# Kernel optimization log

Hardware: AMD Instinct MI355X
Metric: run time of the kernel (lower is better)

## Reference

```python
import jax, jax.numpy as jnp
import numpy as np

D_MODEL = 1024
NUM_HEADS = 16
DEPTH = D_MODEL // NUM_HEADS


def setup_inputs() -> dict:
    key = jax.random.key(0)
    ks = jax.random.split(key, 9)
    s = 1.0 / np.sqrt(D_MODEL)
    x = jax.random.normal(ks[0], (2, 2048, D_MODEL), dtype=jnp.float32)
    def lin(kw, kb):
        W = jax.random.uniform(kw, (D_MODEL, D_MODEL), jnp.float32, -s, s)
        b = jax.random.uniform(kb, (D_MODEL,), jnp.float32, -s, s)
        return W, b
    Wq, bq = lin(ks[1], ks[2])
    Wk, bk = lin(ks[3], ks[4])
    Wv, bv = lin(ks[5], ks[6])
    Wo, bo = lin(ks[7], ks[8])
    return {"x": x, "Wq": Wq, "bq": bq, "Wk": Wk, "bk": bk,
            "Wv": Wv, "bv": bv, "Wo": Wo, "bo": bo}


def reference(x, Wq, bq, Wk, bk, Wv, bv, Wo, bo):
    B, T, _ = x.shape
    # projections; weights stored as [in, out] (torch Linear applies x @ W.T; here W is already [in,out])
    def split_heads(y):
        return y.reshape(B, T, NUM_HEADS, DEPTH).transpose(0, 2, 1, 3)  # [B,H,T,D]
    Q = split_heads(x @ Wq + bq)
    K = split_heads(x @ Wk + bk)
    V = split_heads(x @ Wv + bv)
    scale = 1.0 / jnp.sqrt(jnp.asarray(DEPTH, dtype=x.dtype))
    scores = jnp.einsum('bhqd,bhkd->bhqk', Q, K) * scale  # [B,H,T,T]
    attn = jax.nn.softmax(scores, axis=-1)
    out = jnp.einsum('bhqk,bhkd->bhqd', attn, V)  # [B,H,T,D]
    out = out.transpose(0, 2, 1, 3).reshape(B, T, D_MODEL)
    return out @ Wo + bo
```

## Files before the change

kernel.cpp:

```cpp
#include <hip/hip_runtime.h>
#include <hip/hip_bf16.h>

typedef unsigned short ushort_t;
typedef short s8v __attribute__((ext_vector_type(8)));
typedef float f4v __attribute__((ext_vector_type(4)));
typedef float f16v __attribute__((ext_vector_type(16)));

#define DM 1024
#define TT 2048
#define NH 16
#define DH 64
#define QSCALE 0.18033688011112042f

__device__ __forceinline__ ushort_t f2bf(float f) {
  union { float f; unsigned u; } v; v.f = f;
  unsigned u = v.u;
  return (ushort_t)((u + 0x7fffu + ((u >> 16) & 1u)) >> 16);
}

__device__ __forceinline__ unsigned pk2bf(float a, float b) {
  union { __hip_bfloat162 h; unsigned u; } v;
  v.h = __float22bfloat162_rn(float2{a, b});
  return v.u;
}

__device__ __forceinline__ f16v splat16(float x) {
  f16v v;
#pragma unroll
  for (int i = 0; i < 16; i++) v[i] = x;
  return v;
}

__device__ __forceinline__ void gll16(const void* g, const void* l) {
  __builtin_amdgcn_global_load_lds(
      (const __attribute__((address_space(1))) unsigned int*)g,
      (__attribute__((address_space(3))) unsigned int*)l, 16, 0, 0);
}

__global__ __launch_bounds__(256) void wtrans4_kernel(const float* __restrict__ W0,
                                                      const float* __restrict__ W1,
                                                      const float* __restrict__ W2,
                                                      const float* __restrict__ W3,
                                                      ushort_t* __restrict__ dst) {
  __shared__ float tile[32][33];
  const int z = blockIdx.z;
  const float* W = z == 0 ? W0 : (z == 1 ? W1 : (z == 2 ? W2 : W3));
  ushort_t* Wt = dst + (size_t)z * DM * DM;
  int tx = threadIdx.x & 31, ty = threadIdx.x >> 5;
  int n0 = blockIdx.x * 32, k0 = blockIdx.y * 32;
#pragma unroll
  for (int i = 0; i < 4; i++)
    tile[ty + i * 8][tx] = W[(size_t)(k0 + ty + i * 8) * DM + n0 + tx];
  __syncthreads();
#pragma unroll
  for (int i = 0; i < 4; i++)
    Wt[(size_t)(n0 + ty + i * 8) * DM + k0 + tx] = f2bf(tile[tx][ty + i * 8]);
}

__global__ __launch_bounds__(256) void xconv_kernel(const float* __restrict__ x,
                                                    ushort_t* __restrict__ xb) {
  int i = blockIdx.x * 256 + threadIdx.x;
  const float4* p = (const float4*)x + (size_t)i * 2;
  float4 a = p[0], b = p[1];
  union { ushort_t s[8]; uint4 u; } r;
  r.s[0] = f2bf(a.x); r.s[1] = f2bf(a.y); r.s[2] = f2bf(a.z); r.s[3] = f2bf(a.w);
  r.s[4] = f2bf(b.x); r.s[5] = f2bf(b.y); r.s[6] = f2bf(b.z); r.s[7] = f2bf(b.w);
  *((uint4*)xb + i) = r.u;
}

__global__ __launch_bounds__(256) void vtrans_kernel(const ushort_t* __restrict__ V,
                                                     ushort_t* __restrict__ Vt) {
  __shared__ ushort_t Ls[64][72];
  const int t = threadIdx.x;
  const int t0 = blockIdx.x * 64, bh = blockIdx.y;
  const ushort_t* Vb = V + (size_t)bh * TT * DH;
  ushort_t* Vtb = Vt + (size_t)bh * DH * TT;
#pragma unroll
  for (int c = t; c < 512; c += 256) {
    int tt = c & 63, dch = c >> 6;
    union { uint4 u; ushort_t s[8]; } uu;
    uu.u = *(const uint4*)&Vb[(size_t)(t0 + tt) * DH + dch * 8];
#pragma unroll
    for (int i = 0; i < 8; i++) Ls[dch * 8 + i][tt] = uu.s[i];
  }
  __syncthreads();
#pragma unroll
  for (int c = t; c < 512; c += 256) {
    int d = c >> 3, tch = c & 7;
    uint4 u = *(const uint4*)&Ls[d][tch * 8];
    *(uint4*)&Vtb[(size_t)d * TT + t0 + tch * 8] = u;
  }
}

template <int MT, int MODE>
__global__ __launch_bounds__(256) void gemm_bt(
    const ushort_t* __restrict__ A, const ushort_t* __restrict__ Bt,
    const float* __restrict__ bias0, const float* __restrict__ bias1,
    const float* __restrict__ bias2,
    ushort_t* __restrict__ qo, ushort_t* __restrict__ ko, ushort_t* __restrict__ vo,
    float* __restrict__ co) {
  constexpr int TM = MT * 32;
  __shared__ __align__(16) ushort_t Asm[2][TM * 32];
  __shared__ __align__(16) ushort_t Bsm[2][128 * 32];
  const int m0 = blockIdx.x * TM, n0 = blockIdx.y * 128;
  const int t = threadIdx.x, lane = t & 63;
  const int wid = t >> 6, wr = wid >> 1, wc = wid & 1;
  const ushort_t* Ab = A + (size_t)m0 * DM;
  const ushort_t* Bb = Bt + (size_t)n0 * DM;

  f4v zero = {0.f, 0.f, 0.f, 0.f};
  f4v acc[MT][4];
#pragma unroll
  for (int i = 0; i < MT; i++)
#pragma unroll
    for (int j = 0; j < 4; j++) acc[i][j] = zero;

  const int r0 = t >> 2;
  const int csw = ((t & 3) ^ ((r0 >> 1) & 3)) * 8;
  const int rr = lane & 15, q8 = lane >> 4;

#define GSTAGE(kb, bb)                                                      \
  do {                                                                      \
    int k0_ = (kb) * 32 + csw;                                              \
    gll16(Ab + (size_t)r0 * DM + k0_, &Asm[bb][t * 8]);                     \
    if constexpr (MT == 4)                                                  \
      gll16(Ab + (size_t)(r0 + 64) * DM + k0_, &Asm[bb][(t + 256) * 8]);    \
    gll16(Bb + (size_t)r0 * DM + k0_, &Bsm[bb][t * 8]);                     \
    gll16(Bb + (size_t)(r0 + 64) * DM + k0_, &Bsm[bb][(t + 256) * 8]);      \
  } while (0)

  GSTAGE(0, 0);
  for (int kb = 0; kb < 32; ++kb) {
    const int cur = kb & 1;
    if (kb < 31) {
      GSTAGE(kb + 1, cur ^ 1);
      if constexpr (MT == 4)
        asm volatile("s_waitcnt vmcnt(4)" ::: "memory");
      else
        asm volatile("s_waitcnt vmcnt(3)" ::: "memory");
    } else {
      asm volatile("s_waitcnt vmcnt(0)" ::: "memory");
    }
    __builtin_amdgcn_s_barrier();
    __builtin_amdgcn_sched_barrier(0);

    s8v af[MT], bf_[4];
#pragma unroll
    for (int mt = 0; mt < MT; mt++) {
      int row = wr * (MT * 16) + mt * 16 + rr;
      af[mt] = *(const s8v*)&Asm[cur][row * 32 + ((q8 ^ ((row >> 1) & 3)) << 3)];
    }
#pragma unroll
    for (int nt = 0; nt < 4; nt++) {
      int row = wc * 64 + nt * 16 + rr;
      bf_[nt] = *(const s8v*)&Bsm[cur][row * 32 + ((q8 ^ ((row >> 1) & 3)) << 3)];
    }
    __builtin_amdgcn_s_setprio(1);
#pragma unroll
    for (int mt = 0; mt < MT; mt++)
#pragma unroll
      for (int nt = 0; nt < 4; nt++)
        acc[mt][nt] =
            __builtin_amdgcn_mfma_f32_16x16x32_bf16(af[mt], bf_[nt], acc[mt][nt], 0, 0, 0);
    __builtin_amdgcn_s_setprio(0);
    __builtin_amdgcn_sched_barrier(0);
    __builtin_amdgcn_s_barrier();
  }
#undef GSTAGE

  const int col_l = lane & 15, row_q = (lane >> 4) * 4;
  if (MODE == 0) {
    const int qkv = n0 >> 10;
    const float* bias = qkv == 0 ? bias0 : (qkv == 1 ? bias1 : bias2);
    ushort_t* dst = qkv == 0 ? qo : (qkv == 1 ? ko : vo);
    const float sc = qkv == 0 ? QSCALE : 1.0f;
    const int nb = n0 & 1023;
#pragma unroll
    for (int nt = 0; nt < 4; nt++) {
      int gc = nb + wc * 64 + nt * 16 + col_l;
      float bv_ = bias[gc];
      int hh = gc >> 6, d = gc & 63;
#pragma unroll
      for (int mt = 0; mt < MT; mt++) {
#pragma unroll
        for (int j = 0; j < 4; j++) {
          int r = m0 + wr * (MT * 16) + mt * 16 + row_q + j;
          int bb = r >> 11, tt_ = r & 2047;
          dst[(((size_t)(bb * NH + hh)) * TT + tt_) * DH + d] = f2bf((acc[mt][nt][j] + bv_) * sc);
        }
      }
    }
  } else {
#pragma unroll
    for (int nt = 0; nt < 4; nt++) {
      int gc = n0 + wc * 64 + nt * 16 + col_l;
      float bv_ = bias0[gc];
#pragma unroll
      for (int mt = 0; mt < MT; mt++) {
#pragma unroll
        for (int j = 0; j < 4; j++) {
          int r = m0 + wr * (MT * 16) + mt * 16 + row_q + j;
          co[(size_t)r * DM + gc] = acc[mt][nt][j] + bv_;
        }
      }
    }
  }
}

__global__ __launch_bounds__(256, 2) void attn_kernel(const ushort_t* __restrict__ Q,
                                                      const ushort_t* __restrict__ K,
                                                      const ushort_t* __restrict__ Vt,
                                                      ushort_t* __restrict__ O) {
  __shared__ __align__(16) ushort_t Ksm[2][64 * 64];
  __shared__ __align__(16) ushort_t Vsm[2][64 * 64];

  const int b_lin = blockIdx.x + (blockIdx.y << 4);
  const int xcd = b_lin & 7, n = b_lin >> 3;
  const int bh = (xcd << 2) | (n >> 4);
  const int qt = n & 15;
  const int b = bh >> 4, h = bh & 15;
  const int t = threadIdx.x, lane = t & 63, wid = t >> 6;
  const int lo = lane & 31, hi = lane >> 5;
  const ushort_t* Qb = Q + ((size_t)bh * TT + qt * 128 + wid * 32) * DH;
  const ushort_t* Kb = K + (size_t)bh * TT * DH;
  const ushort_t* Vb = Vt + (size_t)bh * DH * TT;

  s8v qf[4];
#pragma unroll
  for (int ks = 0; ks < 4; ks++)
    qf[ks] = *(const s8v*)&Qb[lo * 64 + ks * 16 + hi * 8];

  f16v oacc[2];
  oacc[0] = splat16(0.f);
  oacc[1] = splat16(0.f);
  float mreg = 0.f, lreg = 0.f;

  const int c0r = t >> 3, c0s = ((t & 7) ^ (c0r & 7)) * 8;
  const int c1 = t + 256;
  const int c1r = c1 >> 3, c1s = ((t & 7) ^ (c1r & 7)) * 8;

#define STAGE(tv, bb)                                              \
  do {                                                             \
    int kv0_ = (tv) * 64;                                          \
    gll16(&Kb[(size_t)(kv0_ + c0r) * DH + c0s], &Ksm[bb][t * 8]);  \
    gll16(&Vb[(size_t)c0r * TT + kv0_ + c0s], &Vsm[bb][t * 8]);    \
    gll16(&Kb[(size_t)(kv0_ + c1r) * DH + c1s], &Ksm[bb][c1 * 8]); \
    gll16(&Vb[(size_t)c1r * TT + kv0_ + c1s], &Vsm[bb][c1 * 8]);   \
  } while (0)

  STAGE(0, 0);
  for (int tv = 0; tv < 32; ++tv) {
    const int cur = tv & 1;
    if (tv < 31) {
      STAGE(tv + 1, cur ^ 1);
      asm volatile("s_waitcnt vmcnt(4)" ::: "memory");
    } else {
      asm volatile("s_waitcnt vmcnt(0)" ::: "memory");
    }
    __builtin_amdgcn_s_barrier();
    __builtin_amdgcn_sched_barrier(0);

    f16v st0 = splat16(-mreg), st1 = splat16(-mreg);
    __builtin_amdgcn_s_setprio(1);
#pragma unroll
    for (int ks = 0; ks < 4; ks++) {
      int ch = ((ks * 2 + hi) ^ (lo & 7)) << 3;
      s8v kf0 = *(const s8v*)&Ksm[cur][lo * 64 + ch];
      s8v kf1 = *(const s8v*)&Ksm[cur][(32 + lo) * 64 + ch];
      st0 = __builtin_amdgcn_mfma_f32_32x32x16_bf16(kf0, qf[ks], st0, 0, 0, 0);
      st1 = __builtin_amdgcn_mfma_f32_32x32x16_bf16(kf1, qf[ks], st1, 0, 0, 0);
    }
    __builtin_amdgcn_s_setprio(0);

    float pmax = -1e30f;
#pragma unroll
    for (int i = 0; i < 16; i++) pmax = fmaxf(pmax, fmaxf(st0[i], st1[i]));
    pmax = fmaxf(pmax, __shfl_xor(pmax, 32, 64));
    if (!__all(pmax <= 8.0f)) {
      float delta = fmaxf(pmax, 0.f);
      float corr = __builtin_amdgcn_exp2f(-delta);
      mreg += delta;
      st0 -= delta;
      st1 -= delta;
      lreg *= corr;
      oacc[0] *= corr;
      oacc[1] *= corr;
    }
#pragma unroll
    for (int i = 0; i < 16; i++) {
      st0[i] = __builtin_amdgcn_exp2f(st0[i]);
      st1[i] = __builtin_amdgcn_exp2f(st1[i]);
    }
    float ps = 0.f;
#pragma unroll
    for (int i = 0; i < 16; i++) ps += st0[i] + st1[i];
    ps += __shfl_xor(ps, 32, 64);
    lreg += ps;

    s8v pb[4];
#pragma unroll
    for (int kt = 0; kt < 2; kt++) {
#pragma unroll
      for (int s = 0; s < 2; s++) {
        unsigned w0, w1, w2, w3;
        if (kt == 0) {
          w0 = pk2bf(st0[8 * s + 0], st0[8 * s + 1]);
          w1 = pk2bf(st0[8 * s + 2], st0[8 * s + 3]);
          w2 = pk2bf(st0[8 * s + 4], st0[8 * s + 5]);
          w3 = pk2bf(st0[8 * s + 6], st0[8 * s + 7]);
        } else {
          w0 = pk2bf(st1[8 * s + 0], st1[8 * s + 1]);
          w1 = pk2bf(st1[8 * s + 2], st1[8 * s + 3]);
          w2 = pk2bf(st1[8 * s + 4], st1[8 * s + 5]);
          w3 = pk2bf(st1[8 * s + 6], st1[8 * s + 7]);
        }
        asm volatile("v_permlane32_swap_b32 %0, %1" : "+v"(w0), "+v"(w2));
        asm volatile("v_permlane32_swap_b32 %0, %1" : "+v"(w1), "+v"(w3));
        union { unsigned u[4]; s8v v; } pw;
        pw.u[0] = w0; pw.u[1] = w1; pw.u[2] = w2; pw.u[3] = w3;
        pb[kt * 2 + s] = pw.v;
      }
    }

    __builtin_amdgcn_s_setprio(1);
#pragma unroll
    for (int ks = 0; ks < 4; ks++) {
      int ch = ((ks * 2 + hi) ^ (lo & 7)) << 3;
      s8v vf0 = *(const s8v*)&Vsm[cur][lo * 64 + ch];
      s8v vf1 = *(const s8v*)&Vsm[cur][(32 + lo) * 64 + ch];
      oacc[0] = __builtin_amdgcn_mfma_f32_32x32x16_bf16(vf0, pb[ks], oacc[0], 0, 0, 0);
      oacc[1] = __builtin_amdgcn_mfma_f32_32x32x16_bf16(vf1, pb[ks], oacc[1], 0, 0, 0);
    }
    __builtin_amdgcn_s_setprio(0);

    __builtin_amdgcn_sched_barrier(0);
    __builtin_amdgcn_s_barrier();
  }
#undef STAGE

  float linv = 1.0f / lreg;
  ushort_t* Osm = &Ksm[0][0] + wid * 2048;
#pragma unroll
  for (int dt = 0; dt < 2; dt++) {
#pragma unroll
    for (int r = 0; r < 8; r++) {
      int dbase = ((2 * r) & 3) + 8 * ((2 * r) >> 2);
      int d = dt * 32 + dbase + 4 * hi;
      unsigned w = pk2bf(oacc[dt][2 * r] * linv, oacc[dt][2 * r + 1] * linv);
      *(unsigned*)&Osm[lo * 64 + (d ^ ((lo & 7) << 3))] = w;
    }
  }
#pragma unroll
  for (int r = 0; r < 4; r++) {
    int q = lane >> 1;
    int chunk = (lane & 1) + r * 2;
    s8v v = *(const s8v*)&Osm[q * 64 + ((chunk ^ (q & 7)) << 3)];
    *(s8v*)&O[((size_t)(b * TT + qt * 128 + wid * 32 + q)) * DM + h * 64 + chunk * 8] = v;
  }
}

extern "C" void kernel_launch(void* const* d_in, const int* in_sizes, int n_in,
                              void* d_out, int out_size, void* d_ws, size_t ws_size,
                              hipStream_t stream) {
  const float* x = (const float*)d_in[0];
  const float* Wq = (const float*)d_in[1];
  const float* bq = (const float*)d_in[2];
  const float* Wk = (const float*)d_in[3];
  const float* bk = (const float*)d_in[4];
  const float* Wv = (const float*)d_in[5];
  const float* bv = (const float*)d_in[6];
  const float* Wo = (const float*)d_in[7];
  const float* bo = (const float*)d_in[8];
  float* out = (float*)d_out;

  char* ws = (char*)d_ws;
  ushort_t* xb = (ushort_t*)(ws);
  ushort_t* wqkv = (ushort_t*)(ws + (8ull << 20));
  ushort_t* wot = (ushort_t*)(ws + (14ull << 20));
  ushort_t* Qb = (ushort_t*)(ws + (16ull << 20));
  ushort_t* Kb = (ushort_t*)(ws + (24ull << 20));
  ushort_t* Vb = (ushort_t*)(ws + (32ull << 20));
  ushort_t* Vtb = xb;
  ushort_t* Ob = Vb;

  dim3 tb(256);
  wtrans4_kernel<<<dim3(32, 32, 4), tb, 0, stream>>>(Wq, Wk, Wv, Wo, wqkv);
  xconv_kernel<<<dim3(2048), tb, 0, stream>>>(x, xb);
  gemm_bt<4, 0><<<dim3(32, 24), tb, 0, stream>>>(xb, wqkv, bq, bk, bv, Qb, Kb, Vb, nullptr);
  vtrans_kernel<<<dim3(32, 32), tb, 0, stream>>>(Vb, Vtb);
  attn_kernel<<<dim3(16, 32), tb, 0, stream>>>(Qb, Kb, Vtb, Ob);
  gemm_bt<2, 1><<<dim3(64, 8), tb, 0, stream>>>(Ob, wot, bo, nullptr, nullptr, nullptr, nullptr,
                                                nullptr, out);
}
```

Before: 208.4 us.

## Split attention over KV halves with combine kernel; merge weight and x conversion

```diff
diff --git a/kernel.cpp b/kernel.cpp
--- a/kernel.cpp
+++ b/kernel.cpp
@@ -18,6 +18,12 @@
   return (ushort_t)((u + 0x7fffu + ((u >> 16) & 1u)) >> 16);
 }
 
+__device__ __forceinline__ float bf2f(ushort_t s) {
+  union { unsigned u; float f; } v;
+  v.u = ((unsigned)s) << 16;
+  return v.f;
+}
+
 __device__ __forceinline__ unsigned pk2bf(float a, float b) {
   union { __hip_bfloat162 h; unsigned u; } v;
   v.h = __float22bfloat162_rn(float2{a, b});
@@ -37,13 +43,29 @@
       (__attribute__((address_space(3))) unsigned int*)l, 16, 0, 0);
 }
 
-__global__ __launch_bounds__(256) void wtrans4_kernel(const float* __restrict__ W0,
-                                                      const float* __restrict__ W1,
-                                                      const float* __restrict__ W2,
-                                                      const float* __restrict__ W3,
-                                                      ushort_t* __restrict__ dst) {
+__global__ __launch_bounds__(256) void prep_kernel(const float* __restrict__ W0,
+                                                   const float* __restrict__ W1,
+                                                   const float* __restrict__ W2,
+                                                   const float* __restrict__ W3,
+                                                   const float* __restrict__ x,
+                                                   ushort_t* __restrict__ dst,
+                                                   ushort_t* __restrict__ xb) {
   __shared__ float tile[32][33];
   const int z = blockIdx.z;
+  if (z == 4) {
+    int lb = blockIdx.y * 32 + blockIdx.x;
+    int i = lb * 256 + threadIdx.x;
+    const float4* p = (const float4*)x + (size_t)i * 4;
+    float4 a = p[0], b = p[1], c = p[2], d = p[3];
+    union { ushort_t s[16]; uint4 u[2]; } r;
+    r.s[0] = f2bf(a.x); r.s[1] = f2bf(a.y); r.s[2] = f2bf(a.z); r.s[3] = f2bf(a.w);
+    r.s[4] = f2bf(b.x); r.s[5] = f2bf(b.y); r.s[6] = f2bf(b.z); r.s[7] = f2bf(b.w);
+    r.s[8] = f2bf(c.x); r.s[9] = f2bf(c.y); r.s[10] = f2bf(c.z); r.s[11] = f2bf(c.w);
+    r.s[12] = f2bf(d.x); r.s[13] = f2bf(d.y); r.s[14] = f2bf(d.z); r.s[15] = f2bf(d.w);
+    ((uint4*)xb)[(size_t)i * 2] = r.u[0];
+    ((uint4*)xb)[(size_t)i * 2 + 1] = r.u[1];
+    return;
+  }
   const float* W = z == 0 ? W0 : (z == 1 ? W1 : (z == 2 ? W2 : W3));
   ushort_t* Wt = dst + (size_t)z * DM * DM;
   int tx = threadIdx.x & 31, ty = threadIdx.x >> 5;
@@ -55,17 +77,6 @@
 #pragma unroll
   for (int i = 0; i < 4; i++)
     Wt[(size_t)(n0 + ty + i * 8) * DM + k0 + tx] = f2bf(tile[tx][ty + i * 8]);
-}
-
-__global__ __launch_bounds__(256) void xconv_kernel(const float* __restrict__ x,
-                                                    ushort_t* __restrict__ xb) {
-  int i = blockIdx.x * 256 + threadIdx.x;
-  const float4* p = (const float4*)x + (size_t)i * 2;
-  float4 a = p[0], b = p[1];
-  union { ushort_t s[8]; uint4 u; } r;
-  r.s[0] = f2bf(a.x); r.s[1] = f2bf(a.y); r.s[2] = f2bf(a.z); r.s[3] = f2bf(a.w);
-  r.s[4] = f2bf(b.x); r.s[5] = f2bf(b.y); r.s[6] = f2bf(b.z); r.s[7] = f2bf(b.w);
-  *((uint4*)xb + i) = r.u;
 }
 
 __global__ __launch_bounds__(256) void vtrans_kernel(const ushort_t* __restrict__ V,
@@ -119,14 +130,14 @@
   const int csw = ((t & 3) ^ ((r0 >> 1) & 3)) * 8;
   const int rr = lane & 15, q8 = lane >> 4;
 
-#define GSTAGE(kb, bb)                                                      \
-  do {                                                                      \
-    int k0_ = (kb) * 32 + csw;                                              \
-    gll16(Ab + (size_t)r0 * DM + k0_, &Asm[bb][t * 8]);                     \
-    if constexpr (MT == 4)                                                  \
-      gll16(Ab + (size_t)(r0 + 64) * DM + k0_, &Asm[bb][(t + 256) * 8]);    \
-    gll16(Bb + (size_t)r0 * DM + k0_, &Bsm[bb][t * 8]);                     \
-    gll16(Bb + (size_t)(r0 + 64) * DM + k0_, &Bsm[bb][(t + 256) * 8]);      \
+#define GSTAGE(kb, bb)                                                   \
+  do {                                                                   \
+    int k0_ = (kb) * 32 + csw;                                           \
+    gll16(Ab + (size_t)r0 * DM + k0_, &Asm[bb][t * 8]);                  \
+    if constexpr (MT == 4)                                               \
+      gll16(Ab + (size_t)(r0 + 64) * DM + k0_, &Asm[bb][(t + 256) * 8]); \
+    gll16(Bb + (size_t)r0 * DM + k0_, &Bsm[bb][t * 8]);                  \
+    gll16(Bb + (size_t)(r0 + 64) * DM + k0_, &Bsm[bb][(t + 256) * 8]);   \
   } while (0)
 
   GSTAGE(0, 0);
@@ -207,10 +218,11 @@
   }
 }
 
-__global__ __launch_bounds__(256, 2) void attn_kernel(const ushort_t* __restrict__ Q,
+__global__ __launch_bounds__(256, 4) void attn_kernel(const ushort_t* __restrict__ Q,
                                                       const ushort_t* __restrict__ K,
                                                       const ushort_t* __restrict__ Vt,
-                                                      ushort_t* __restrict__ O) {
+                                                      ushort_t* __restrict__ Opart,
+                                                      float2* __restrict__ stats, int ntiles) {
   __shared__ __align__(16) ushort_t Ksm[2][64 * 64];
   __shared__ __align__(16) ushort_t Vsm[2][64 * 64];
 
@@ -218,12 +230,14 @@
   const int xcd = b_lin & 7, n = b_lin >> 3;
   const int bh = (xcd << 2) | (n >> 4);
   const int qt = n & 15;
+  const int z = blockIdx.z;
   const int b = bh >> 4, h = bh & 15;
   const int t = threadIdx.x, lane = t & 63, wid = t >> 6;
   const int lo = lane & 31, hi = lane >> 5;
   const ushort_t* Qb = Q + ((size_t)bh * TT + qt * 128 + wid * 32) * DH;
   const ushort_t* Kb = K + (size_t)bh * TT * DH;
   const ushort_t* Vb = Vt + (size_t)bh * DH * TT;
+  ushort_t* Op = Opart + (size_t)z * (2 * TT) * DM;
 
   s8v qf[4];
 #pragma unroll
@@ -238,6 +252,7 @@
   const int c0r = t >> 3, c0s = ((t & 7) ^ (c0r & 7)) * 8;
   const int c1 = t + 256;
   const int c1r = c1 >> 3, c1s = ((t & 7) ^ (c1r & 7)) * 8;
+  const int tv0 = z * ntiles;
 
 #define STAGE(tv, bb)                                              \
   do {                                                             \
@@ -248,11 +263,11 @@
     gll16(&Vb[(size_t)c1r * TT + kv0_ + c1s], &Vsm[bb][c1 * 8]);   \
   } while (0)
 
-  STAGE(0, 0);
-  for (int tv = 0; tv < 32; ++tv) {
-    const int cur = tv & 1;
-    if (tv < 31) {
-      STAGE(tv + 1, cur ^ 1);
+  STAGE(tv0, 0);
+  for (int it = 0; it < ntiles; ++it) {
+    const int cur = it & 1;
+    if (it < ntiles - 1) {
+      STAGE(tv0 + it + 1, cur ^ 1);
       asm volatile("s_waitcnt vmcnt(4)" ::: "memory");
     } else {
       asm volatile("s_waitcnt vmcnt(0)" ::: "memory");
@@ -338,7 +353,11 @@
   }
 #undef STAGE
 
-  float linv = 1.0f / lreg;
+  if (hi == 0) {
+    int qrow = qt * 128 + wid * 32 + lo;
+    stats[((size_t)(z * 32 + bh)) * TT + qrow] = float2{mreg, lreg};
+  }
+
   ushort_t* Osm = &Ksm[0][0] + wid * 2048;
 #pragma unroll
   for (int dt = 0; dt < 2; dt++) {
@@ -346,7 +365,7 @@
     for (int r = 0; r < 8; r++) {
       int dbase = ((2 * r) & 3) + 8 * ((2 * r) >> 2);
       int d = dt * 32 + dbase + 4 * hi;
-      unsigned w = pk2bf(oacc[dt][2 * r] * linv, oacc[dt][2 * r + 1] * linv);
+      unsigned w = pk2bf(oacc[dt][2 * r], oacc[dt][2 * r + 1]);
       *(unsigned*)&Osm[lo * 64 + (d ^ ((lo & 7) << 3))] = w;
     }
   }
@@ -355,8 +374,36 @@
     int q = lane >> 1;
     int chunk = (lane & 1) + r * 2;
     s8v v = *(const s8v*)&Osm[q * 64 + ((chunk ^ (q & 7)) << 3)];
-    *(s8v*)&O[((size_t)(b * TT + qt * 128 + wid * 32 + q)) * DM + h * 64 + chunk * 8] = v;
-  }
+    *(s8v*)&Op[((size_t)(b * TT + qt * 128 + wid * 32 + q)) * DM + h * 64 + chunk * 8] = v;
+  }
+}
+
+__global__ __launch_bounds__(256) void combine_kernel(const ushort_t* __restrict__ Opart,
+                                                      const float2* __restrict__ stats,
+                                                      ushort_t* __restrict__ O, int nsplit) {
+  int i = blockIdx.x * 256 + threadIdx.x;
+  int bt = i >> 7, c = i & 127;
+  int b = bt >> 11, t = bt & 2047;
+  int bh = b * NH + (c >> 3);
+  float2 s0 = stats[(size_t)bh * TT + t];
+  union { uint4 u; ushort_t s[8]; } p0, p1, r;
+  p0.u = *((const uint4*)Opart + i);
+  if (nsplit == 2) {
+    float2 s1 = stats[(size_t)(32 + bh) * TT + t];
+    p1.u = *((const uint4*)(Opart + (size_t)(2 * TT) * DM) + i);
+    float ms = fmaxf(s0.x, s1.x);
+    float w0 = __builtin_amdgcn_exp2f(s0.x - ms);
+    float w1 = __builtin_amdgcn_exp2f(s1.x - ms);
+    float inv = 1.0f / (w0 * s0.y + w1 * s1.y);
+#pragma unroll
+    for (int j = 0; j < 8; j++)
+      r.s[j] = f2bf((w0 * bf2f(p0.s[j]) + w1 * bf2f(p1.s[j])) * inv);
+  } else {
+    float inv = 1.0f / s0.y;
+#pragma unroll
+    for (int j = 0; j < 8; j++) r.s[j] = f2bf(bf2f(p0.s[j]) * inv);
+  }
+  *((uint4*)O + i) = r.u;
 }
 
 extern "C" void kernel_launch(void* const* d_in, const int* in_sizes, int n_in,
@@ -381,14 +428,18 @@
   ushort_t* Kb = (ushort_t*)(ws + (24ull << 20));
   ushort_t* Vb = (ushort_t*)(ws + (32ull << 20));
   ushort_t* Vtb = xb;
-  ushort_t* Ob = Vb;
+  ushort_t* Opart = Vb;
+  ushort_t* Ob = Qb;
+
+  const int nsplit = (ws_size >= (49ull << 20)) ? 2 : 1;
+  float2* stats = (float2*)(ws + ((nsplit == 2 ? 48ull : 40ull) << 20));
 
   dim3 tb(256);
-  wtrans4_kernel<<<dim3(32, 32, 4), tb, 0, stream>>>(Wq, Wk, Wv, Wo, wqkv);
-  xconv_kernel<<<dim3(2048), tb, 0, stream>>>(x, xb);
+  prep_kernel<<<dim3(32, 32, 5), tb, 0, stream>>>(Wq, Wk, Wv, Wo, x, wqkv, xb);
   gemm_bt<4, 0><<<dim3(32, 24), tb, 0, stream>>>(xb, wqkv, bq, bk, bv, Qb, Kb, Vb, nullptr);
   vtrans_kernel<<<dim3(32, 32), tb, 0, stream>>>(Vb, Vtb);
-  attn_kernel<<<dim3(16, 32), tb, 0, stream>>>(Qb, Kb, Vtb, Ob);
+  attn_kernel<<<dim3(16, 32, nsplit), tb, 0, stream>>>(Qb, Kb, Vtb, Opart, stats, 32 / nsplit);
+  combine_kernel<<<dim3(2048), tb, 0, stream>>>(Opart, stats, Ob, nsplit);
   gemm_bt<2, 1><<<dim3(64, 8), tb, 0, stream>>>(Ob, wot, bo, nullptr, nullptr, nullptr, nullptr,
                                                 nullptr, out);
 }
```

Result: no change. 208.4 us (+0.0%).
